# Optimization experiments

Measured on AMD Instinct MI355X. Metric: run time of the kernel, lower is better.

The kernel has to match this reference:

```python
import jax, jax.numpy as jnp
import numpy as np

N_NODES = 50000
N_EDGES = 800000
IN_F = 256
HID = 64
N_CLASSES = 32
LEAKY_SLOPE = 0.2


def _gat_layer(x, src, dst, W, a_src, a_dst):
    # Standard single-head GAT (GraphAttentionLayer_P0 semantics):
    # h = x W; e_ij = LeakyReLU(a_src.h_j + a_dst.h_i); softmax over in-edges of i;
    # out_i = sum_j alpha_ij h_j
    h = x @ W                                        # [N, F']
    alpha_s = h @ a_src                              # [N]
    alpha_d = h @ a_dst                              # [N]
    e = jax.nn.leaky_relu(alpha_s[src] + alpha_d[dst], LEAKY_SLOPE)  # [E]
    # segment softmax over edges grouped by destination node
    m = jax.ops.segment_max(e, dst, num_segments=N_NODES)           # [N]
    m = jnp.where(jnp.isfinite(m), m, 0.0)            # empty segments -> -inf
    ex = jnp.exp(e - m[dst])                          # [E]
    denom = jax.ops.segment_sum(ex, dst, num_segments=N_NODES)       # [N]
    denom = jnp.where(denom == 0.0, 1.0, denom)
    alpha = ex / denom[dst]                           # [E]
    out = jax.ops.segment_sum(alpha[:, None] * h[src], dst, num_segments=N_NODES)
    return out                                        # [N, F']


def setup_inputs() -> dict:
    key = jax.random.key(0)
    ks = jax.random.split(key, 8)
    x = jax.random.normal(ks[0], (N_NODES, IN_F), dtype=jnp.float32)
    edge_index = jax.random.randint(ks[1], (2, N_EDGES), 0, N_NODES, dtype=jnp.int64)
    s1 = 1.0 / np.sqrt(IN_F)
    s2 = 1.0 / np.sqrt(HID)
    W1 = jax.random.uniform(ks[2], (IN_F, HID), jnp.float32, -s1, s1)
    a1_src = jax.random.uniform(ks[3], (HID,), jnp.float32, -s2, s2)
    a1_dst = jax.random.uniform(ks[4], (HID,), jnp.float32, -s2, s2)
    W2 = jax.random.uniform(ks[5], (HID, N_CLASSES), jnp.float32, -s2, s2)
    s3 = 1.0 / np.sqrt(N_CLASSES)
    a2_src = jax.random.uniform(ks[6], (N_CLASSES,), jnp.float32, -s3, s3)
    a2_dst = jax.random.uniform(ks[7], (N_CLASSES,), jnp.float32, -s3, s3)
    return {"x": x, "edge_index": edge_index, "W1": W1, "a1_src": a1_src,
            "a1_dst": a1_dst, "W2": W2, "a2_src": a2_src, "a2_dst": a2_dst}


def reference(x, edge_index, W1, a1_src, a1_dst, W2, a2_src, a2_dst):
    src, dst = edge_index[0], edge_index[1]
    h = _gat_layer(x, src, dst, W1, a1_src, a1_dst)
    h = jax.nn.relu(h)
    out = _gat_layer(h, src, dst, W2, a2_src, a2_dst)
    return out
```

## Files before the change

### kernel.cpp

```cpp
#include <hip/hip_runtime.h>
#include <math.h>

#define NN 50000
#define NE 800000
#define INF_DIM 256
#define HIDF 64
#define NC 32
#define SLOPE 0.2f


__global__ void k_zero(int* __restrict__ counts){
  int i = blockIdx.x*blockDim.x + threadIdx.x;
  if(i < NN) counts[i] = 0;
}

__global__ void k_hist(const int* __restrict__ dst, int* __restrict__ counts){
  int e = blockIdx.x*blockDim.x + threadIdx.x;
  if(e < NE) atomicAdd(&counts[dst[e]], 1);
}

__global__ void k_scan_a(const int* __restrict__ counts, int* __restrict__ rowstart,
                         int* __restrict__ blocksums){
  __shared__ int wsum[4];
  int tid = threadIdx.x;
  int idx = blockIdx.x*1024 + tid*4;
  int v0 = (idx+0<NN)?counts[idx+0]:0;
  int v1 = (idx+1<NN)?counts[idx+1]:0;
  int v2 = (idx+2<NN)?counts[idx+2]:0;
  int v3 = (idx+3<NN)?counts[idx+3]:0;
  int s0=v0, s1=s0+v1, s2=s1+v2, s3=s2+v3;
  int lane = tid & 63, w = tid >> 6;
  int x = s3;
  #pragma unroll
  for(int off=1; off<64; off<<=1){
    int y = __shfl_up(x, off, 64);
    if(lane >= off) x += y;
  }
  if(lane==63) wsum[w] = x;
  __syncthreads();
  int woff = 0;
  for(int i=0;i<w;i++) woff += wsum[i];
  int excl = woff + (x - s3);
  if(idx+0<NN) rowstart[idx+1] = excl + s0;
  if(idx+1<NN) rowstart[idx+2] = excl + s1;
  if(idx+2<NN) rowstart[idx+3] = excl + s2;
  if(idx+3<NN) rowstart[idx+4] = excl + s3;
  if(tid==0) blocksums[blockIdx.x] = wsum[0]+wsum[1]+wsum[2]+wsum[3];
}

__global__ void k_scan_b(const int* __restrict__ blocksums, int* __restrict__ blockoff){
  int lane = threadIdx.x;
  const int nb = (NN + 1023)/1024;
  int v = (lane<nb)? blocksums[lane] : 0;
  int x = v;
  #pragma unroll
  for(int off=1; off<64; off<<=1){
    int y = __shfl_up(x, off, 64);
    if(lane >= off) x += y;
  }
  if(lane<nb) blockoff[lane] = x - v;
}

__global__ void k_scan_c(const int* __restrict__ counts, int* __restrict__ rowstart,
                         const int* __restrict__ blockoff, int* __restrict__ cursor){
  int i = blockIdx.x*blockDim.x + threadIdx.x;
  if(i < NN){
    int incl = rowstart[i+1] + blockoff[i>>10];
    rowstart[i+1] = incl;
    cursor[i] = incl - counts[i];
    if(i==0) rowstart[0] = 0;
  }
}

__global__ void k_scatter(const int* __restrict__ src, const int* __restrict__ dst,
                          int* __restrict__ cursor, int* __restrict__ ssrc){
  int e = blockIdx.x*blockDim.x + threadIdx.x;
  if(e < NE){
    int d = dst[e];
    int pos = atomicAdd(&cursor[d], 1);
    ssrc[pos] = src[e];
  }
}


__global__ __launch_bounds__(64) void k_gemm1(
    const float* __restrict__ x, const float* __restrict__ W,
    const float* __restrict__ a_s, const float* __restrict__ a_d,
    float* __restrict__ h, float* __restrict__ as_o, float* __restrict__ ad_o){
  __shared__ float ws[8*64];
  float4* wsv = reinterpret_cast<float4*>(ws);
  const float4* Wv = reinterpret_cast<const float4*>(W);
  int tid = threadIdx.x;
  int ng = tid >> 3, cg = tid & 7;
  int nb0 = blockIdx.x*32;

  const float* xrow[4];
  #pragma unroll
  for(int i=0;i<4;i++){
    int n = nb0 + ng + 8*i;
    xrow[i] = x + (size_t)((n < NN) ? n : (NN-1))*INF_DIM;
  }

  float4 acc[4][2];
  #pragma unroll
  for(int i=0;i<4;i++){ acc[i][0]=make_float4(0.f,0.f,0.f,0.f); acc[i][1]=make_float4(0.f,0.f,0.f,0.f); }

  for(int st=0; st<32; ++st){
    int k0 = st*8;
    wsv[tid]      = Wv[k0*16 + tid];
    wsv[tid + 64] = Wv[k0*16 + 64 + tid];
    float4 xa[4][2];
    #pragma unroll
    for(int i=0;i<4;i++){
      xa[i][0] = *reinterpret_cast<const float4*>(xrow[i] + k0);
      xa[i][1] = *reinterpret_cast<const float4*>(xrow[i] + k0 + 4);
    }
    __syncthreads();
    #pragma unroll
    for(int k4=0;k4<2;k4++){
      float4 wf[4][2];
      #pragma unroll
      for(int kk=0;kk<4;kk++){
        wf[kk][0] = wsv[(k4*4+kk)*16 + cg*2];
        wf[kk][1] = wsv[(k4*4+kk)*16 + cg*2 + 1];
      }
      #pragma unroll
      for(int i=0;i<4;i++){
        float4 xv = xa[i][k4];
        acc[i][0].x += xv.x*wf[0][0].x + xv.y*wf[1][0].x + xv.z*wf[2][0].x + xv.w*wf[3][0].x;
        acc[i][0].y += xv.x*wf[0][0].y + xv.y*wf[1][0].y + xv.z*wf[2][0].y + xv.w*wf[3][0].y;
        acc[i][0].z += xv.x*wf[0][0].z + xv.y*wf[1][0].z + xv.z*wf[2][0].z + xv.w*wf[3][0].z;
        acc[i][0].w += xv.x*wf[0][0].w + xv.y*wf[1][0].w + xv.z*wf[2][0].w + xv.w*wf[3][0].w;
        acc[i][1].x += xv.x*wf[0][1].x + xv.y*wf[1][1].x + xv.z*wf[2][1].x + xv.w*wf[3][1].x;
        acc[i][1].y += xv.x*wf[0][1].y + xv.y*wf[1][1].y + xv.z*wf[2][1].y + xv.w*wf[3][1].y;
        acc[i][1].z += xv.x*wf[0][1].z + xv.y*wf[1][1].z + xv.z*wf[2][1].z + xv.w*wf[3][1].z;
        acc[i][1].w += xv.x*wf[0][1].w + xv.y*wf[1][1].w + xv.z*wf[2][1].w + xv.w*wf[3][1].w;
      }
    }
    __syncthreads();
  }

  const float4* asv = reinterpret_cast<const float4*>(a_s);
  const float4* adv = reinterpret_cast<const float4*>(a_d);
  float4 asA = asv[cg*2], asB = asv[cg*2+1];
  float4 adA = adv[cg*2], adB = adv[cg*2+1];
  #pragma unroll
  for(int i=0;i<4;i++){
    int n = nb0 + ng + 8*i;
    float sv = acc[i][0].x*asA.x + acc[i][0].y*asA.y + acc[i][0].z*asA.z + acc[i][0].w*asA.w
             + acc[i][1].x*asB.x + acc[i][1].y*asB.y + acc[i][1].z*asB.z + acc[i][1].w*asB.w;
    float dv = acc[i][0].x*adA.x + acc[i][0].y*adA.y + acc[i][0].z*adA.z + acc[i][0].w*adA.w
             + acc[i][1].x*adB.x + acc[i][1].y*adB.y + acc[i][1].z*adB.z + acc[i][1].w*adB.w;
    #pragma unroll
    for(int mk=1; mk<8; mk<<=1){
      sv += __shfl_xor(sv, mk, 64);
      dv += __shfl_xor(dv, mk, 64);
    }
    if(n < NN){
      *reinterpret_cast<float4*>(h + (size_t)n*HIDF + cg*8)     = acc[i][0];
      *reinterpret_cast<float4*>(h + (size_t)n*HIDF + cg*8 + 4) = acc[i][1];
      if(cg==0){ as_o[n]=sv; ad_o[n]=dv; }
    }
  }
}


__global__ __launch_bounds__(256) void k_agg1(
    const float* __restrict__ h1, const float* __restrict__ as1, const float* __restrict__ ad1,
    const int* __restrict__ rowstart, const int* __restrict__ ssrc,
    float* __restrict__ r1){
  int lane = threadIdx.x & 63;
  int n = blockIdx.x*4 + (threadIdx.x >> 6);
  int rs = rowstart[n], re = rowstart[n+1];
  float adn = ad1[n];
  float m = -1e30f, l = 0.f, acc = 0.f;
  for(int base=rs; base<re; base+=64){
    int cnt = re - base; if(cnt > 64) cnt = 64;
    int s = 0; float z = -1e30f;
    if(lane < cnt){
      s = ssrc[base+lane];
      float zz = as1[s] + adn;
      z = zz > 0.f ? zz : SLOPE*zz;
    }
    float cm = z;
    #pragma unroll
    for(int off=32; off>=1; off>>=1) cm = fmaxf(cm, __shfl_xor(cm, off, 64));
    float nm = fmaxf(m, cm);
    float sc = __expf(m - nm);
    float p = (lane<cnt) ? __expf(z - nm) : 0.f;
    float cs = p;
    #pragma unroll
    for(int off=32; off>=1; off>>=1) cs += __shfl_xor(cs, off, 64);
    l = l*sc + cs;
    acc *= sc;
    int e = 0;
    for(; e+4<=cnt; e+=4){
      int   se0 = __shfl(s, e,   64), se1 = __shfl(s, e+1, 64);
      int   se2 = __shfl(s, e+2, 64), se3 = __shfl(s, e+3, 64);
      float pe0 = __shfl(p, e,   64), pe1 = __shfl(p, e+1, 64);
      float pe2 = __shfl(p, e+2, 64), pe3 = __shfl(p, e+3, 64);
      float v0 = h1[(size_t)se0*HIDF + lane];
      float v1 = h1[(size_t)se1*HIDF + lane];
      float v2 = h1[(size_t)se2*HIDF + lane];
      float v3 = h1[(size_t)se3*HIDF + lane];
      acc += pe0*v0; acc += pe1*v1; acc += pe2*v2; acc += pe3*v3;
    }
    for(; e<cnt; ++e){
      int   se = __shfl(s, e, 64);
      float pe = __shfl(p, e, 64);
      acc += pe * h1[(size_t)se*HIDF + lane];
    }
    m = nm;
  }
  float o = (l > 0.f) ? acc/l : 0.f;
  r1[(size_t)n*HIDF + lane] = fmaxf(o, 0.f);
}


__global__ __launch_bounds__(64) void k_gemm2(
    const float* __restrict__ r1, const float* __restrict__ W2,
    const float* __restrict__ a_s, const float* __restrict__ a_d,
    float* __restrict__ h2, float* __restrict__ as_o, float* __restrict__ ad_o){
  __shared__ float ws2[64*32];
  float4* wsv = reinterpret_cast<float4*>(ws2);
  const float4* Wv = reinterpret_cast<const float4*>(W2);
  int tid = threadIdx.x;
  int ng = tid >> 3, cg = tid & 7;
  int nb0 = blockIdx.x*32;
  #pragma unroll
  for(int j=0;j<8;j++) wsv[j*64 + tid] = Wv[j*64 + tid];

  const float* xrow[4];
  #pragma unroll
  for(int i=0;i<4;i++){
    int n = nb0 + ng + 8*i;
    xrow[i] = r1 + (size_t)((n < NN) ? n : (NN-1))*HIDF;
  }
  float4 acc[4];
  #pragma unroll
  for(int i=0;i<4;i++) acc[i] = make_float4(0.f,0.f,0.f,0.f);
  __syncthreads();

  for(int st=0; st<8; ++st){
    int k0 = st*8;
    float4 xa[4][2];
    #pragma unroll
    for(int i=0;i<4;i++){
      xa[i][0] = *reinterpret_cast<const float4*>(xrow[i] + k0);
      xa[i][1] = *reinterpret_cast<const float4*>(xrow[i] + k0 + 4);
    }
    #pragma unroll
    for(int k4=0;k4<2;k4++){
      float4 wf[4];
      #pragma unroll
      for(int kk=0;kk<4;kk++) wf[kk] = wsv[(k0 + k4*4 + kk)*8 + cg];
      #pragma unroll
      for(int i=0;i<4;i++){
        float4 xv = xa[i][k4];
        acc[i].x += xv.x*wf[0].x + xv.y*wf[1].x + xv.z*wf[2].x + xv.w*wf[3].x;
        acc[i].y += xv.x*wf[0].y + xv.y*wf[1].y + xv.z*wf[2].y + xv.w*wf[3].y;
        acc[i].z += xv.x*wf[0].z + xv.y*wf[1].z + xv.z*wf[2].z + xv.w*wf[3].z;
        acc[i].w += xv.x*wf[0].w + xv.y*wf[1].w + xv.z*wf[2].w + xv.w*wf[3].w;
      }
    }
  }

  const float4* asv = reinterpret_cast<const float4*>(a_s);
  const float4* adv = reinterpret_cast<const float4*>(a_d);
  float4 as4 = asv[cg], ad4 = adv[cg];
  #pragma unroll
  for(int i=0;i<4;i++){
    int n = nb0 + ng + 8*i;
    float sv = acc[i].x*as4.x + acc[i].y*as4.y + acc[i].z*as4.z + acc[i].w*as4.w;
    float dv = acc[i].x*ad4.x + acc[i].y*ad4.y + acc[i].z*ad4.z + acc[i].w*ad4.w;
    #pragma unroll
    for(int mk=1; mk<8; mk<<=1){
      sv += __shfl_xor(sv, mk, 64);
      dv += __shfl_xor(dv, mk, 64);
    }
    if(n < NN){
      *reinterpret_cast<float4*>(h2 + (size_t)n*NC + cg*4) = acc[i];
      if(cg==0){ as_o[n]=sv; ad_o[n]=dv; }
    }
  }
}


__global__ __launch_bounds__(256) void k_agg2(
    const float* __restrict__ h2, const float* __restrict__ as2, const float* __restrict__ ad2,
    const int* __restrict__ rowstart, const int* __restrict__ ssrc,
    float* __restrict__ out){
  int tid = threadIdx.x;
  int c = tid & 31;
  int n = blockIdx.x*8 + (tid >> 5);
  int rs = rowstart[n], re = rowstart[n+1];
  float adn = ad2[n];
  float m = -1e30f, l = 0.f, acc = 0.f;
  for(int base=rs; base<re; base+=32){
    int cnt = re - base; if(cnt > 32) cnt = 32;
    int s = 0; float z = -1e30f;
    if(c < cnt){
      s = ssrc[base+c];
      float zz = as2[s] + adn;
      z = zz > 0.f ? zz : SLOPE*zz;
    }
    float cm = z;
    #pragma unroll
    for(int off=16; off>=1; off>>=1) cm = fmaxf(cm, __shfl_xor(cm, off, 32));
    float nm = fmaxf(m, cm);
    float sc = __expf(m - nm);
    float p = (c<cnt) ? __expf(z - nm) : 0.f;
    float cs = p;
    #pragma unroll
    for(int off=16; off>=1; off>>=1) cs += __shfl_xor(cs, off, 32);
    l = l*sc + cs;
    acc *= sc;
    int e = 0;
    for(; e+4<=cnt; e+=4){
      int   se0 = __shfl(s, e,   32), se1 = __shfl(s, e+1, 32);
      int   se2 = __shfl(s, e+2, 32), se3 = __shfl(s, e+3, 32);
      float pe0 = __shfl(p, e,   32), pe1 = __shfl(p, e+1, 32);
      float pe2 = __shfl(p, e+2, 32), pe3 = __shfl(p, e+3, 32);
      float v0 = h2[(size_t)se0*NC + c];
      float v1 = h2[(size_t)se1*NC + c];
      float v2 = h2[(size_t)se2*NC + c];
      float v3 = h2[(size_t)se3*NC + c];
      acc += pe0*v0; acc += pe1*v1; acc += pe2*v2; acc += pe3*v3;
    }
    for(; e<cnt; ++e){
      int   se = __shfl(s, e, 32);
      float pe = __shfl(p, e, 32);
      acc += pe * h2[(size_t)se*NC + c];
    }
    m = nm;
  }
  out[(size_t)n*NC + c] = (l > 0.f) ? acc/l : 0.f;
}


extern "C" void kernel_launch(void* const* d_in, const int* in_sizes, int n_in,
                              void* d_out, int out_size, void* d_ws, size_t ws_size,
                              hipStream_t stream){
  const float* x   = (const float*)d_in[0];
  const int*   ei  = (const int*)d_in[1];
  const float* W1  = (const float*)d_in[2];
  const float* a1s = (const float*)d_in[3];
  const float* a1d = (const float*)d_in[4];
  const float* W2  = (const float*)d_in[5];
  const float* a2s = (const float*)d_in[6];
  const float* a2d = (const float*)d_in[7];
  const int* srcIdx = ei;
  const int* dstIdx = ei + NE;
  float* out = (float*)d_out;

  char* wsp = (char*)d_ws;
  size_t off = 0;
  auto alloc = [&](size_t bytes)->void*{
    void* p = wsp + off;
    off = (off + bytes + 255) & ~(size_t)255;
    return p;
  };
  int* counts    = (int*)alloc((size_t)NN*sizeof(int));
  int* rowstart  = (int*)alloc((size_t)(NN+1)*sizeof(int));
  int* cursor    = (int*)alloc((size_t)NN*sizeof(int));
  int* blocksums = (int*)alloc(64*sizeof(int));
  int* blockoff  = (int*)alloc(64*sizeof(int));
  int* ssrc      = (int*)alloc((size_t)NE*sizeof(int));
  float* h1      = (float*)alloc((size_t)NN*HIDF*sizeof(float));
  float* as1     = (float*)alloc((size_t)NN*sizeof(float));
  float* ad1     = (float*)alloc((size_t)NN*sizeof(float));
  float* r1      = (float*)alloc((size_t)NN*HIDF*sizeof(float));
  float* h2  = h1;
  float* as2 = as1;
  float* ad2 = ad1;

  k_zero   <<<(NN+255)/256, 256, 0, stream>>>(counts);
  k_hist   <<<(NE+255)/256, 256, 0, stream>>>(dstIdx, counts);
  k_scan_a <<<(NN+1023)/1024, 256, 0, stream>>>(counts, rowstart, blocksums);
  k_scan_b <<<1, 64, 0, stream>>>(blocksums, blockoff);
  k_scan_c <<<(NN+255)/256, 256, 0, stream>>>(counts, rowstart, blockoff, cursor);
  k_scatter<<<(NE+255)/256, 256, 0, stream>>>(srcIdx, dstIdx, cursor, ssrc);

  k_gemm1<<<(NN+31)/32, 64, 0, stream>>>(x, W1, a1s, a1d, h1, as1, ad1);
  k_agg1 <<<NN/4, 256, 0, stream>>>(h1, as1, ad1, rowstart, ssrc, r1);

  k_gemm2<<<(NN+31)/32, 64, 0, stream>>>(r1, W2, a2s, a2d, h2, as2, ad2);
  k_agg2 <<<NN/8, 256, 0, stream>>>(h2, as2, ad2, rowstart, ssrc, out);
}
```

Before: 302.7 us.

## Rewrite projection GEMMs with register-prefetched weights instead of shared memory

Both dense projection kernels drop the shared-memory weight staging and its barriers. Each thread now reads its weight slice straight from global or cache into a rotating register window, and prefetches x rows two steps ahead in double-buffered registers. Blocks now cover 16 nodes instead of 32, which doubles the grid but halves the rows each thread handles. This removes syncthreads stalls but adds redundant global weight loads per wave, and the extra clamped loads at the end of the weight stream could raise cache traffic.

```diff
diff --git a/kernel.cpp b/kernel.cpp
--- a/kernel.cpp
+++ b/kernel.cpp
@@ -7,6 +7,14 @@
 #define HIDF 64
 #define NC 32
 #define SLOPE 0.2f
+
+__device__ __forceinline__ float elem8(const float4& a, const float4& b, int kk){
+  switch(kk){
+    case 0: return a.x; case 1: return a.y; case 2: return a.z; case 3: return a.w;
+    case 4: return b.x; case 5: return b.y; case 6: return b.z; default: return b.w;
+  }
+}
+#define FMA4(A,S,V) {A.x += (S)*(V).x; A.y += (S)*(V).y; A.z += (S)*(V).z; A.w += (S)*(V).w;}
 
 
 __global__ void k_zero(int* __restrict__ counts){
@@ -87,80 +95,84 @@
     const float* __restrict__ x, const float* __restrict__ W,
     const float* __restrict__ a_s, const float* __restrict__ a_d,
     float* __restrict__ h, float* __restrict__ as_o, float* __restrict__ ad_o){
-  __shared__ float ws[8*64];
-  float4* wsv = reinterpret_cast<float4*>(ws);
-  const float4* Wv = reinterpret_cast<const float4*>(W);
-  int tid = threadIdx.x;
-  int ng = tid >> 3, cg = tid & 7;
-  int nb0 = blockIdx.x*32;
-
-  const float* xrow[4];
-  #pragma unroll
-  for(int i=0;i<4;i++){
-    int n = nb0 + ng + 8*i;
-    xrow[i] = x + (size_t)((n < NN) ? n : (NN-1))*INF_DIM;
-  }
-
-  float4 acc[4][2];
-  #pragma unroll
-  for(int i=0;i<4;i++){ acc[i][0]=make_float4(0.f,0.f,0.f,0.f); acc[i][1]=make_float4(0.f,0.f,0.f,0.f); }
-
+  int lane = threadIdx.x;
+  int cg = lane & 7;
+  int ng = lane >> 3;
+  int nb0 = blockIdx.x*16;
+  int n0 = nb0 + ng, n1 = nb0 + ng + 8;
+  const float* xr0 = x + (size_t)(n0 < NN ? n0 : NN-1)*INF_DIM;
+  const float* xr1 = x + (size_t)(n1 < NN ? n1 : NN-1)*INF_DIM;
+  const float* wp = W + cg*8;
+
+  float4 acc00 = make_float4(0.f,0.f,0.f,0.f), acc01 = acc00;
+  float4 acc10 = acc00, acc11 = acc00;
+
+  float4 xs[2][2][2];
+  float4 wr[4][2];
+
+  #pragma unroll
+  for(int s=0;s<2;s++){
+    xs[s][0][0] = *(const float4*)(xr0 + s*8);
+    xs[s][0][1] = *(const float4*)(xr0 + s*8 + 4);
+    xs[s][1][0] = *(const float4*)(xr1 + s*8);
+    xs[s][1][1] = *(const float4*)(xr1 + s*8 + 4);
+  }
+  #pragma unroll
+  for(int r=0;r<4;r++){
+    wr[r][0] = *(const float4*)(wp + r*64);
+    wr[r][1] = *(const float4*)(wp + r*64 + 4);
+  }
+
+  #pragma unroll 2
   for(int st=0; st<32; ++st){
-    int k0 = st*8;
-    wsv[tid]      = Wv[k0*16 + tid];
-    wsv[tid + 64] = Wv[k0*16 + 64 + tid];
-    float4 xa[4][2];
-    #pragma unroll
-    for(int i=0;i<4;i++){
-      xa[i][0] = *reinterpret_cast<const float4*>(xrow[i] + k0);
-      xa[i][1] = *reinterpret_cast<const float4*>(xrow[i] + k0 + 4);
-    }
-    __syncthreads();
-    #pragma unroll
-    for(int k4=0;k4<2;k4++){
-      float4 wf[4][2];
-      #pragma unroll
-      for(int kk=0;kk<4;kk++){
-        wf[kk][0] = wsv[(k4*4+kk)*16 + cg*2];
-        wf[kk][1] = wsv[(k4*4+kk)*16 + cg*2 + 1];
-      }
-      #pragma unroll
-      for(int i=0;i<4;i++){
-        float4 xv = xa[i][k4];
-        acc[i][0].x += xv.x*wf[0][0].x + xv.y*wf[1][0].x + xv.z*wf[2][0].x + xv.w*wf[3][0].x;
-        acc[i][0].y += xv.x*wf[0][0].y + xv.y*wf[1][0].y + xv.z*wf[2][0].y + xv.w*wf[3][0].y;
-        acc[i][0].z += xv.x*wf[0][0].z + xv.y*wf[1][0].z + xv.z*wf[2][0].z + xv.w*wf[3][0].z;
-        acc[i][0].w += xv.x*wf[0][0].w + xv.y*wf[1][0].w + xv.z*wf[2][0].w + xv.w*wf[3][0].w;
-        acc[i][1].x += xv.x*wf[0][1].x + xv.y*wf[1][1].x + xv.z*wf[2][1].x + xv.w*wf[3][1].x;
-        acc[i][1].y += xv.x*wf[0][1].y + xv.y*wf[1][1].y + xv.z*wf[2][1].y + xv.w*wf[3][1].y;
-        acc[i][1].z += xv.x*wf[0][1].z + xv.y*wf[1][1].z + xv.z*wf[2][1].z + xv.w*wf[3][1].z;
-        acc[i][1].w += xv.x*wf[0][1].w + xv.y*wf[1][1].w + xv.z*wf[2][1].w + xv.w*wf[3][1].w;
-      }
-    }
-    __syncthreads();
-  }
-
-  const float4* asv = reinterpret_cast<const float4*>(a_s);
-  const float4* adv = reinterpret_cast<const float4*>(a_d);
-  float4 asA = asv[cg*2], asB = asv[cg*2+1];
-  float4 adA = adv[cg*2], adB = adv[cg*2+1];
-  #pragma unroll
-  for(int i=0;i<4;i++){
-    int n = nb0 + ng + 8*i;
-    float sv = acc[i][0].x*asA.x + acc[i][0].y*asA.y + acc[i][0].z*asA.z + acc[i][0].w*asA.w
-             + acc[i][1].x*asB.x + acc[i][1].y*asB.y + acc[i][1].z*asB.z + acc[i][1].w*asB.w;
-    float dv = acc[i][0].x*adA.x + acc[i][0].y*adA.y + acc[i][0].z*adA.z + acc[i][0].w*adA.w
-             + acc[i][1].x*adB.x + acc[i][1].y*adB.y + acc[i][1].z*adB.z + acc[i][1].w*adB.w;
-    #pragma unroll
-    for(int mk=1; mk<8; mk<<=1){
-      sv += __shfl_xor(sv, mk, 64);
-      dv += __shfl_xor(dv, mk, 64);
-    }
-    if(n < NN){
-      *reinterpret_cast<float4*>(h + (size_t)n*HIDF + cg*8)     = acc[i][0];
-      *reinterpret_cast<float4*>(h + (size_t)n*HIDF + cg*8 + 4) = acc[i][1];
-      if(cg==0){ as_o[n]=sv; ad_o[n]=dv; }
-    }
+    int buf = st & 1;
+    #pragma unroll
+    for(int kk=0; kk<8; ++kk){
+      float xk0 = elem8(xs[buf][0][0], xs[buf][0][1], kk);
+      float xk1 = elem8(xs[buf][1][0], xs[buf][1][1], kk);
+      float4 wa = wr[kk & 3][0];
+      float4 wb = wr[kk & 3][1];
+      FMA4(acc00, xk0, wa) FMA4(acc01, xk0, wb)
+      FMA4(acc10, xk1, wa) FMA4(acc11, xk1, wb)
+      int knext = st*8 + kk + 4; if(knext > 255) knext = 255;
+      wr[kk & 3][0] = *(const float4*)(wp + knext*64);
+      wr[kk & 3][1] = *(const float4*)(wp + knext*64 + 4);
+    }
+    int sn = st + 2;
+    if(sn < 32){
+      xs[buf][0][0] = *(const float4*)(xr0 + sn*8);
+      xs[buf][0][1] = *(const float4*)(xr0 + sn*8 + 4);
+      xs[buf][1][0] = *(const float4*)(xr1 + sn*8);
+      xs[buf][1][1] = *(const float4*)(xr1 + sn*8 + 4);
+    }
+  }
+
+  float4 asA = *(const float4*)(a_s + cg*8), asB = *(const float4*)(a_s + cg*8 + 4);
+  float4 adA = *(const float4*)(a_d + cg*8), adB = *(const float4*)(a_d + cg*8 + 4);
+  float sv0 = acc00.x*asA.x + acc00.y*asA.y + acc00.z*asA.z + acc00.w*asA.w
+            + acc01.x*asB.x + acc01.y*asB.y + acc01.z*asB.z + acc01.w*asB.w;
+  float dv0 = acc00.x*adA.x + acc00.y*adA.y + acc00.z*adA.z + acc00.w*adA.w
+            + acc01.x*adB.x + acc01.y*adB.y + acc01.z*adB.z + acc01.w*adB.w;
+  float sv1 = acc10.x*asA.x + acc10.y*asA.y + acc10.z*asA.z + acc10.w*asA.w
+            + acc11.x*asB.x + acc11.y*asB.y + acc11.z*asB.z + acc11.w*asB.w;
+  float dv1 = acc10.x*adA.x + acc10.y*adA.y + acc10.z*adA.z + acc10.w*adA.w
+            + acc11.x*adB.x + acc11.y*adB.y + acc11.z*adB.z + acc11.w*adB.w;
+  #pragma unroll
+  for(int mk=1; mk<8; mk<<=1){
+    sv0 += __shfl_xor(sv0, mk, 64);
+    dv0 += __shfl_xor(dv0, mk, 64);
+    sv1 += __shfl_xor(sv1, mk, 64);
+    dv1 += __shfl_xor(dv1, mk, 64);
+  }
+  if(n0 < NN){
+    *(float4*)(h + (size_t)n0*HIDF + cg*8)     = acc00;
+    *(float4*)(h + (size_t)n0*HIDF + cg*8 + 4) = acc01;
+    if(cg==0){ as_o[n0]=sv0; ad_o[n0]=dv0; }
+  }
+  if(n1 < NN){
+    *(float4*)(h + (size_t)n1*HIDF + cg*8)     = acc10;
+    *(float4*)(h + (size_t)n1*HIDF + cg*8 + 4) = acc11;
+    if(cg==0){ as_o[n1]=sv1; ad_o[n1]=dv1; }
   }
 }
 
@@ -221,67 +233,63 @@
     const float* __restrict__ r1, const float* __restrict__ W2,
     const float* __restrict__ a_s, const float* __restrict__ a_d,
     float* __restrict__ h2, float* __restrict__ as_o, float* __restrict__ ad_o){
-  __shared__ float ws2[64*32];
-  float4* wsv = reinterpret_cast<float4*>(ws2);
-  const float4* Wv = reinterpret_cast<const float4*>(W2);
-  int tid = threadIdx.x;
-  int ng = tid >> 3, cg = tid & 7;
-  int nb0 = blockIdx.x*32;
-  #pragma unroll
-  for(int j=0;j<8;j++) wsv[j*64 + tid] = Wv[j*64 + tid];
-
-  const float* xrow[4];
-  #pragma unroll
-  for(int i=0;i<4;i++){
-    int n = nb0 + ng + 8*i;
-    xrow[i] = r1 + (size_t)((n < NN) ? n : (NN-1))*HIDF;
-  }
-  float4 acc[4];
-  #pragma unroll
-  for(int i=0;i<4;i++) acc[i] = make_float4(0.f,0.f,0.f,0.f);
-  __syncthreads();
-
+  int lane = threadIdx.x;
+  int cg = lane & 3;
+  int ng = lane >> 2;
+  int n = blockIdx.x*16 + ng;
+  const float* xrow = r1 + (size_t)(n < NN ? n : NN-1)*HIDF;
+  const float* wp = W2 + cg*8;
+
+  float4 acc0 = make_float4(0.f,0.f,0.f,0.f), acc1 = acc0;
+  float4 xs[2][2];
+  float4 wr[4][2];
+
+  #pragma unroll
+  for(int s=0;s<2;s++){
+    xs[s][0] = *(const float4*)(xrow + s*8);
+    xs[s][1] = *(const float4*)(xrow + s*8 + 4);
+  }
+  #pragma unroll
+  for(int r=0;r<4;r++){
+    wr[r][0] = *(const float4*)(wp + r*32);
+    wr[r][1] = *(const float4*)(wp + r*32 + 4);
+  }
+
+  #pragma unroll 2
   for(int st=0; st<8; ++st){
-    int k0 = st*8;
-    float4 xa[4][2];
-    #pragma unroll
-    for(int i=0;i<4;i++){
-      xa[i][0] = *reinterpret_cast<const float4*>(xrow[i] + k0);
-      xa[i][1] = *reinterpret_cast<const float4*>(xrow[i] + k0 + 4);
-    }
-    #pragma unroll
-    for(int k4=0;k4<2;k4++){
-      float4 wf[4];
-      #pragma unroll
-      for(int kk=0;kk<4;kk++) wf[kk] = wsv[(k0 + k4*4 + kk)*8 + cg];
-      #pragma unroll
-      for(int i=0;i<4;i++){
-        float4 xv = xa[i][k4];
-        acc[i].x += xv.x*wf[0].x + xv.y*wf[1].x + xv.z*wf[2].x + xv.w*wf[3].x;
-        acc[i].y += xv.x*wf[0].y + xv.y*wf[1].y + xv.z*wf[2].y + xv.w*wf[3].y;
-        acc[i].z += xv.x*wf[0].z + xv.y*wf[1].z + xv.z*wf[2].z + xv.w*wf[3].z;
-        acc[i].w += xv.x*wf[0].w + xv.y*wf[1].w + xv.z*wf[2].w + xv.w*wf[3].w;
-      }
-    }
-  }
-
-  const float4* asv = reinterpret_cast<const float4*>(a_s);
-  const float4* adv = reinterpret_cast<const float4*>(a_d);
-  float4 as4 = asv[cg], ad4 = adv[cg];
-  #pragma unroll
-  for(int i=0;i<4;i++){
-    int n = nb0 + ng + 8*i;
-    float sv = acc[i].x*as4.x + acc[i].y*as4.y + acc[i].z*as4.z + acc[i].w*as4.w;
-    float dv = acc[i].x*ad4.x + acc[i].y*ad4.y + acc[i].z*ad4.z + acc[i].w*ad4.w;
-    #pragma unroll
-    for(int mk=1; mk<8; mk<<=1){
-      sv += __shfl_xor(sv, mk, 64);
-      dv += __shfl_xor(dv, mk, 64);
-    }
-    if(n < NN){
-      *reinterpret_cast<float4*>(h2 + (size_t)n*NC + cg*4) = acc[i];
-      if(cg==0){ as_o[n]=sv; ad_o[n]=dv; }
-    }
+    int buf = st & 1;
+    #pragma unroll
+    for(int kk=0; kk<8; ++kk){
+      float xk = elem8(xs[buf][0], xs[buf][1], kk);
+      float4 wa = wr[kk & 3][0];
+      float4 wb = wr[kk & 3][1];
+      FMA4(acc0, xk, wa) FMA4(acc1, xk, wb)
+      int knext = st*8 + kk + 4; if(knext > 63) knext = 63;
+      wr[kk & 3][0] = *(const float4*)(wp + knext*32);
+      wr[kk & 3][1] = *(const float4*)(wp + knext*32 + 4);
+    }
+    int sn = st + 2;
+    if(sn < 8){
+      xs[buf][0] = *(const float4*)(xrow + sn*8);
+      xs[buf][1] = *(const float4*)(xrow + sn*8 + 4);
+    }
+  }
+
+  float4 asA = *(const float4*)(a_s + cg*8), asB = *(const float4*)(a_s + cg*8 + 4);
+  float4 adA = *(const float4*)(a_d + cg*8), adB = *(const float4*)(a_d + cg*8 + 4);
+  float sv = acc0.x*asA.x + acc0.y*asA.y + acc0.z*asA.z + acc0.w*asA.w
+           + acc1.x*asB.x + acc1.y*asB.y + acc1.z*asB.z + acc1.w*asB.w;
+  float dv = acc0.x*adA.x + acc0.y*adA.y + acc0.z*adA.z + acc0.w*adA.w
+           + acc1.x*adB.x + acc1.y*adB.y + acc1.z*adB.z + acc1.w*adB.w;
+  #pragma unroll
+  for(int mk=1; mk<4; mk<<=1){
+    sv += __shfl_xor(sv, mk, 64);
+    dv += __shfl_xor(dv, mk, 64);
+  }
+  if(n < NN){
+    *(float4*)(h2 + (size_t)n*NC + cg*8)     = acc0;
+    *(float4*)(h2 + (size_t)n*NC + cg*8 + 4) = acc1;
+    if(cg==0){ as_o[n]=sv; ad_o[n]=dv; }
   }
 }
 
@@ -381,9 +389,9 @@
   k_scan_c <<<(NN+255)/256, 256, 0, stream>>>(counts, rowstart, blockoff, cursor);
   k_scatter<<<(NE+255)/256, 256, 0, stream>>>(srcIdx, dstIdx, cursor, ssrc);
 
-  k_gemm1<<<(NN+31)/32, 64, 0, stream>>>(x, W1, a1s, a1d, h1, as1, ad1);
+  k_gemm1<<<(NN+15)/16, 64, 0, stream>>>(x, W1, a1s, a1d, h1, as1, ad1);
   k_agg1 <<<NN/4, 256, 0, stream>>>(h1, as1, ad1, rowstart, ssrc, r1);
 
-  k_gemm2<<<(NN+31)/32, 64, 0, stream>>>(r1, W2, a2s, a2d, h2, as2, ad2);
+  k_gemm2<<<(NN+15)/16, 64, 0, stream>>>(r1, W2, a2s, a2d, h2, as2, ad2);
   k_agg2 <<<NN/8, 256, 0, stream>>>(h2, as2, ad2, rowstart, ssrc, out);
 }
```

Result: slower. 346.5 us (+14.5%).

## Restructure both GEMMs to one output column per lane with register double-buffering

Applied to the files above, without the earlier changes.

Both projection GEMMs are rewritten so each lane owns one output column and accumulates 8 node rows. X rows are broadcast float4 loads shared across the wavefront, and W columns are read directly from global memory, replacing the LDS staging and its barriers. The next k-slice is prefetched into registers while the current one is computed. This removes shared-memory traffic and syncs, but makes the attention dot-products use full-wave shuffle reductions and relies on NN being divisible by 8 and 16.

```diff
diff --git a/kernel.cpp b/kernel.cpp
--- a/kernel.cpp
+++ b/kernel.cpp
@@ -7,6 +7,10 @@
 #define HIDF 64
 #define NC 32
 #define SLOPE 0.2f
+
+__device__ __forceinline__ float elem4(const float4& v, int kk){
+  switch(kk){ case 0: return v.x; case 1: return v.y; case 2: return v.z; default: return v.w; }
+}
 
 
 __global__ void k_zero(int* __restrict__ counts){
@@ -87,80 +91,53 @@
     const float* __restrict__ x, const float* __restrict__ W,
     const float* __restrict__ a_s, const float* __restrict__ a_d,
     float* __restrict__ h, float* __restrict__ as_o, float* __restrict__ ad_o){
-  __shared__ float ws[8*64];
-  float4* wsv = reinterpret_cast<float4*>(ws);
-  const float4* Wv = reinterpret_cast<const float4*>(W);
-  int tid = threadIdx.x;
-  int ng = tid >> 3, cg = tid & 7;
-  int nb0 = blockIdx.x*32;
-
-  const float* xrow[4];
-  #pragma unroll
-  for(int i=0;i<4;i++){
-    int n = nb0 + ng + 8*i;
-    xrow[i] = x + (size_t)((n < NN) ? n : (NN-1))*INF_DIM;
-  }
-
-  float4 acc[4][2];
-  #pragma unroll
-  for(int i=0;i<4;i++){ acc[i][0]=make_float4(0.f,0.f,0.f,0.f); acc[i][1]=make_float4(0.f,0.f,0.f,0.f); }
-
-  for(int st=0; st<32; ++st){
-    int k0 = st*8;
-    wsv[tid]      = Wv[k0*16 + tid];
-    wsv[tid + 64] = Wv[k0*16 + 64 + tid];
-    float4 xa[4][2];
-    #pragma unroll
-    for(int i=0;i<4;i++){
-      xa[i][0] = *reinterpret_cast<const float4*>(xrow[i] + k0);
-      xa[i][1] = *reinterpret_cast<const float4*>(xrow[i] + k0 + 4);
-    }
-    __syncthreads();
-    #pragma unroll
-    for(int k4=0;k4<2;k4++){
-      float4 wf[4][2];
-      #pragma unroll
-      for(int kk=0;kk<4;kk++){
-        wf[kk][0] = wsv[(k4*4+kk)*16 + cg*2];
-        wf[kk][1] = wsv[(k4*4+kk)*16 + cg*2 + 1];
-      }
-      #pragma unroll
-      for(int i=0;i<4;i++){
-        float4 xv = xa[i][k4];
-        acc[i][0].x += xv.x*wf[0][0].x + xv.y*wf[1][0].x + xv.z*wf[2][0].x + xv.w*wf[3][0].x;
-        acc[i][0].y += xv.x*wf[0][0].y + xv.y*wf[1][0].y + xv.z*wf[2][0].y + xv.w*wf[3][0].y;
-        acc[i][0].z += xv.x*wf[0][0].z + xv.y*wf[1][0].z + xv.z*wf[2][0].z + xv.w*wf[3][0].z;
-        acc[i][0].w += xv.x*wf[0][0].w + xv.y*wf[1][0].w + xv.z*wf[2][0].w + xv.w*wf[3][0].w;
-        acc[i][1].x += xv.x*wf[0][1].x + xv.y*wf[1][1].x + xv.z*wf[2][1].x + xv.w*wf[3][1].x;
-        acc[i][1].y += xv.x*wf[0][1].y + xv.y*wf[1][1].y + xv.z*wf[2][1].y + xv.w*wf[3][1].y;
-        acc[i][1].z += xv.x*wf[0][1].z + xv.y*wf[1][1].z + xv.z*wf[2][1].z + xv.w*wf[3][1].z;
-        acc[i][1].w += xv.x*wf[0][1].w + xv.y*wf[1][1].w + xv.z*wf[2][1].w + xv.w*wf[3][1].w;
-      }
-    }
-    __syncthreads();
-  }
-
-  const float4* asv = reinterpret_cast<const float4*>(a_s);
-  const float4* adv = reinterpret_cast<const float4*>(a_d);
-  float4 asA = asv[cg*2], asB = asv[cg*2+1];
-  float4 adA = adv[cg*2], adB = adv[cg*2+1];
-  #pragma unroll
-  for(int i=0;i<4;i++){
-    int n = nb0 + ng + 8*i;
-    float sv = acc[i][0].x*asA.x + acc[i][0].y*asA.y + acc[i][0].z*asA.z + acc[i][0].w*asA.w
-             + acc[i][1].x*asB.x + acc[i][1].y*asB.y + acc[i][1].z*asB.z + acc[i][1].w*asB.w;
-    float dv = acc[i][0].x*adA.x + acc[i][0].y*adA.y + acc[i][0].z*adA.z + acc[i][0].w*adA.w
-             + acc[i][1].x*adB.x + acc[i][1].y*adB.y + acc[i][1].z*adB.z + acc[i][1].w*adB.w;
-    #pragma unroll
-    for(int mk=1; mk<8; mk<<=1){
+  int c = threadIdx.x;
+  int nb = blockIdx.x*8;
+  const float* wc = W + c;
+
+  float acc[8];
+  #pragma unroll
+  for(int i=0;i<8;i++) acc[i] = 0.f;
+
+  float4 xs[2][8];
+  float  wr[2][4];
+
+  #pragma unroll
+  for(int i=0;i<8;i++) xs[0][i] = *(const float4*)(x + (size_t)(nb+i)*INF_DIM);
+  #pragma unroll
+  for(int kk=0;kk<4;kk++) wr[0][kk] = wc[kk*64];
+
+  #pragma unroll 2
+  for(int st=0; st<64; ++st){
+    int buf = st & 1, nxt = buf ^ 1;
+    if(st < 63){
+      int k0 = (st+1)*4;
+      #pragma unroll
+      for(int i=0;i<8;i++)
+        xs[nxt][i] = *(const float4*)(x + (size_t)(nb+i)*INF_DIM + k0);
+      #pragma unroll
+      for(int kk=0;kk<4;kk++) wr[nxt][kk] = wc[(k0+kk)*64];
+    }
+    #pragma unroll
+    for(int kk=0;kk<4;kk++){
+      float w = wr[buf][kk];
+      #pragma unroll
+      for(int i=0;i<8;i++) acc[i] += elem4(xs[buf][i], kk) * w;
+    }
+  }
+
+  float asc = a_s[c], adc = a_d[c];
+  #pragma unroll
+  for(int i=0;i<8;i++){
+    int n = nb + i;
+    h[(size_t)n*HIDF + c] = acc[i];
+    float sv = acc[i]*asc, dv = acc[i]*adc;
+    #pragma unroll
+    for(int mk=1; mk<64; mk<<=1){
       sv += __shfl_xor(sv, mk, 64);
       dv += __shfl_xor(dv, mk, 64);
     }
-    if(n < NN){
-      *reinterpret_cast<float4*>(h + (size_t)n*HIDF + cg*8)     = acc[i][0];
-      *reinterpret_cast<float4*>(h + (size_t)n*HIDF + cg*8 + 4) = acc[i][1];
-      if(cg==0){ as_o[n]=sv; ad_o[n]=dv; }
-    }
+    if(c==0){ as_o[n]=sv; ad_o[n]=dv; }
   }
 }
 
@@ -221,67 +198,55 @@
     const float* __restrict__ r1, const float* __restrict__ W2,
     const float* __restrict__ a_s, const float* __restrict__ a_d,
     float* __restrict__ h2, float* __restrict__ as_o, float* __restrict__ ad_o){
-  __shared__ float ws2[64*32];
-  float4* wsv = reinterpret_cast<float4*>(ws2);
-  const float4* Wv = reinterpret_cast<const float4*>(W2);
-  int tid = threadIdx.x;
-  int ng = tid >> 3, cg = tid & 7;
-  int nb0 = blockIdx.x*32;
-  #pragma unroll
-  for(int j=0;j<8;j++) wsv[j*64 + tid] = Wv[j*64 + tid];
-
-  const float* xrow[4];
-  #pragma unroll
-  for(int i=0;i<4;i++){
-    int n = nb0 + ng + 8*i;
-    xrow[i] = r1 + (size_t)((n < NN) ? n : (NN-1))*HIDF;
-  }
-  float4 acc[4];
-  #pragma unroll
-  for(int i=0;i<4;i++) acc[i] = make_float4(0.f,0.f,0.f,0.f);
-  __syncthreads();
-
-  for(int st=0; st<8; ++st){
-    int k0 = st*8;
-    float4 xa[4][2];
-    #pragma unroll
-    for(int i=0;i<4;i++){
-      xa[i][0] = *reinterpret_cast<const float4*>(xrow[i] + k0);
-      xa[i][1] = *reinterpret_cast<const float4*>(xrow[i] + k0 + 4);
-    }
-    #pragma unroll
-    for(int k4=0;k4<2;k4++){
-      float4 wf[4];
-      #pragma unroll
-      for(int kk=0;kk<4;kk++) wf[kk] = wsv[(k0 + k4*4 + kk)*8 + cg];
-      #pragma unroll
-      for(int i=0;i<4;i++){
-        float4 xv = xa[i][k4];
-        acc[i].x += xv.x*wf[0].x + xv.y*wf[1].x + xv.z*wf[2].x + xv.w*wf[3].x;
-        acc[i].y += xv.x*wf[0].y + xv.y*wf[1].y + xv.z*wf[2].y + xv.w*wf[3].y;
-        acc[i].z += xv.x*wf[0].z + xv.y*wf[1].z + xv.z*wf[2].z + xv.w*wf[3].z;
-        acc[i].w += xv.x*wf[0].w + xv.y*wf[1].w + xv.z*wf[2].w + xv.w*wf[3].w;
-      }
-    }
-  }
-
-  const float4* asv = reinterpret_cast<const float4*>(a_s);
-  const float4* adv = reinterpret_cast<const float4*>(a_d);
-  float4 as4 = asv[cg], ad4 = adv[cg];
-  #pragma unroll
-  for(int i=0;i<4;i++){
-    int n = nb0 + ng + 8*i;
-    float sv = acc[i].x*as4.x + acc[i].y*as4.y + acc[i].z*as4.z + acc[i].w*as4.w;
-    float dv = acc[i].x*ad4.x + acc[i].y*ad4.y + acc[i].z*ad4.z + acc[i].w*ad4.w;
-    #pragma unroll
-    for(int mk=1; mk<8; mk<<=1){
+  int lane = threadIdx.x;
+  int c = lane & 31;
+  int g = lane >> 5;
+  int nb = blockIdx.x*16 + g*8;
+  const float* wc = W2 + c;
+
+  float acc[8];
+  #pragma unroll
+  for(int i=0;i<8;i++) acc[i] = 0.f;
+
+  float4 xs[2][8];
+  float  wr[2][4];
+
+  #pragma unroll
+  for(int i=0;i<8;i++) xs[0][i] = *(const float4*)(r1 + (size_t)(nb+i)*HIDF);
+  #pragma unroll
+  for(int kk=0;kk<4;kk++) wr[0][kk] = wc[kk*32];
+
+  #pragma unroll 2
+  for(int st=0; st<16; ++st){
+    int buf = st & 1, nxt = buf ^ 1;
+    if(st < 15){
+      int k0 = (st+1)*4;
+      #pragma unroll
+      for(int i=0;i<8;i++)
+        xs[nxt][i] = *(const float4*)(r1 + (size_t)(nb+i)*HIDF + k0);
+      #pragma unroll
+      for(int kk=0;kk<4;kk++) wr[nxt][kk] = wc[(k0+kk)*32];
+    }
+    #pragma unroll
+    for(int kk=0;kk<4;kk++){
+      float w = wr[buf][kk];
+      #pragma unroll
+      for(int i=0;i<8;i++) acc[i] += elem4(xs[buf][i], kk) * w;
+    }
+  }
+
+  float asc = a_s[c], adc = a_d[c];
+  #pragma unroll
+  for(int i=0;i<8;i++){
+    int n = nb + i;
+    h2[(size_t)n*NC + c] = acc[i];
+    float sv = acc[i]*asc, dv = acc[i]*adc;
+    #pragma unroll
+    for(int mk=1; mk<32; mk<<=1){
       sv += __shfl_xor(sv, mk, 64);
       dv += __shfl_xor(dv, mk, 64);
     }
-    if(n < NN){
-      *reinterpret_cast<float4*>(h2 + (size_t)n*NC + cg*4) = acc[i];
-      if(cg==0){ as_o[n]=sv; ad_o[n]=dv; }
-    }
+    if(c==0){ as_o[n]=sv; ad_o[n]=dv; }
   }
 }
 
@@ -381,9 +346,9 @@
   k_scan_c <<<(NN+255)/256, 256, 0, stream>>>(counts, rowstart, blockoff, cursor);
   k_scatter<<<(NE+255)/256, 256, 0, stream>>>(srcIdx, dstIdx, cursor, ssrc);
 
-  k_gemm1<<<(NN+31)/32, 64, 0, stream>>>(x, W1, a1s, a1d, h1, as1, ad1);
+  k_gemm1<<<NN/8, 64, 0, stream>>>(x, W1, a1s, a1d, h1, as1, ad1);
   k_agg1 <<<NN/4, 256, 0, stream>>>(h1, as1, ad1, rowstart, ssrc, r1);
 
-  k_gemm2<<<(NN+31)/32, 64, 0, stream>>>(r1, W2, a2s, a2d, h2, as2, ad2);
+  k_gemm2<<<NN/16, 64, 0, stream>>>(r1, W2, a2s, a2d, h2, as2, ad2);
   k_agg2 <<<NN/8, 256, 0, stream>>>(h2, as2, ad2, rowstart, ssrc, out);
 }
```

Result: slower. 388.2 us (+28.2%).

## Double-buffer GEMM tiles, prefetch x rows, and unroll aggregation gathers by eight

Applied to the files above, without the earlier changes.

k_gemm1 now keeps two W tiles in LDS and loads the next one while computing on the current one. It drops both __syncthreads, on the basis that the 64-thread block is a single wave64. Both GEMMs also prefetch x rows two K-steps ahead in registers, and their dot products are rewritten as explicit scalar-times-vector FMAs. The aggregation kernels unroll the neighbor gather loop from 4 to 8 so more independent loads are in flight, at the cost of extra registers and a longer scalar tail loop.

```diff
diff --git a/kernel.cpp b/kernel.cpp
--- a/kernel.cpp
+++ b/kernel.cpp
@@ -7,6 +7,11 @@
 #define HIDF 64
 #define NC 32
 #define SLOPE 0.2f
+
+__device__ __forceinline__ float elem4(const float4& v, int kk){
+  switch(kk){ case 0: return v.x; case 1: return v.y; case 2: return v.z; default: return v.w; }
+}
+#define FMA4(A,S,V) {A.x += (S)*(V).x; A.y += (S)*(V).y; A.z += (S)*(V).z; A.w += (S)*(V).w;}
 
 
 __global__ void k_zero(int* __restrict__ counts){
@@ -87,7 +92,7 @@
     const float* __restrict__ x, const float* __restrict__ W,
     const float* __restrict__ a_s, const float* __restrict__ a_d,
     float* __restrict__ h, float* __restrict__ as_o, float* __restrict__ ad_o){
-  __shared__ float ws[8*64];
+  __shared__ float ws[2*8*64];
   float4* wsv = reinterpret_cast<float4*>(ws);
   const float4* Wv = reinterpret_cast<const float4*>(W);
   int tid = threadIdx.x;
@@ -105,39 +110,55 @@
   #pragma unroll
   for(int i=0;i<4;i++){ acc[i][0]=make_float4(0.f,0.f,0.f,0.f); acc[i][1]=make_float4(0.f,0.f,0.f,0.f); }
 
+  {
+    float4 wa = Wv[tid], wb = Wv[64+tid];
+    wsv[tid] = wa; wsv[64+tid] = wb;
+  }
+  float4 xs[2][4][2];
+  #pragma unroll
+  for(int i=0;i<4;i++){
+    xs[0][i][0] = *(const float4*)(xrow[i]);
+    xs[0][i][1] = *(const float4*)(xrow[i] + 4);
+    xs[1][i][0] = *(const float4*)(xrow[i] + 8);
+    xs[1][i][1] = *(const float4*)(xrow[i] + 12);
+  }
+
+  #pragma unroll 2
   for(int st=0; st<32; ++st){
-    int k0 = st*8;
-    wsv[tid]      = Wv[k0*16 + tid];
-    wsv[tid + 64] = Wv[k0*16 + 64 + tid];
-    float4 xa[4][2];
-    #pragma unroll
-    for(int i=0;i<4;i++){
-      xa[i][0] = *reinterpret_cast<const float4*>(xrow[i] + k0);
-      xa[i][1] = *reinterpret_cast<const float4*>(xrow[i] + k0 + 4);
-    }
-    __syncthreads();
-    #pragma unroll
-    for(int k4=0;k4<2;k4++){
+    int cur = st & 1, nxt = cur ^ 1;
+    if(st < 31){
+      float4 wa = Wv[(st+1)*128 + tid];
+      float4 wb = Wv[(st+1)*128 + 64 + tid];
+      wsv[nxt*128 + tid] = wa;
+      wsv[nxt*128 + 64 + tid] = wb;
+    }
+    #pragma unroll
+    for(int g=0; g<2; ++g){
       float4 wf[4][2];
       #pragma unroll
       for(int kk=0;kk<4;kk++){
-        wf[kk][0] = wsv[(k4*4+kk)*16 + cg*2];
-        wf[kk][1] = wsv[(k4*4+kk)*16 + cg*2 + 1];
+        wf[kk][0] = wsv[cur*128 + (g*4+kk)*16 + cg*2];
+        wf[kk][1] = wsv[cur*128 + (g*4+kk)*16 + cg*2 + 1];
       }
       #pragma unroll
       for(int i=0;i<4;i++){
-        float4 xv = xa[i][k4];
-        acc[i][0].x += xv.x*wf[0][0].x + xv.y*wf[1][0].x + xv.z*wf[2][0].x + xv.w*wf[3][0].x;
-        acc[i][0].y += xv.x*wf[0][0].y + xv.y*wf[1][0].y + xv.z*wf[2][0].y + xv.w*wf[3][0].y;
-        acc[i][0].z += xv.x*wf[0][0].z + xv.y*wf[1][0].z + xv.z*wf[2][0].z + xv.w*wf[3][0].z;
-        acc[i][0].w += xv.x*wf[0][0].w + xv.y*wf[1][0].w + xv.z*wf[2][0].w + xv.w*wf[3][0].w;
-        acc[i][1].x += xv.x*wf[0][1].x + xv.y*wf[1][1].x + xv.z*wf[2][1].x + xv.w*wf[3][1].x;
-        acc[i][1].y += xv.x*wf[0][1].y + xv.y*wf[1][1].y + xv.z*wf[2][1].y + xv.w*wf[3][1].y;
-        acc[i][1].z += xv.x*wf[0][1].z + xv.y*wf[1][1].z + xv.z*wf[2][1].z + xv.w*wf[3][1].z;
-        acc[i][1].w += xv.x*wf[0][1].w + xv.y*wf[1][1].w + xv.z*wf[2][1].w + xv.w*wf[3][1].w;
+        float4 xv = xs[cur][i][g];
+        #pragma unroll
+        for(int kk=0;kk<4;kk++){
+          float xk = elem4(xv, kk);
+          FMA4(acc[i][0], xk, wf[kk][0])
+          FMA4(acc[i][1], xk, wf[kk][1])
+        }
       }
     }
-    __syncthreads();
+    if(st < 30){
+      int k0 = (st+2)*8;
+      #pragma unroll
+      for(int i=0;i<4;i++){
+        xs[cur][i][0] = *(const float4*)(xrow[i] + k0);
+        xs[cur][i][1] = *(const float4*)(xrow[i] + k0 + 4);
+      }
+    }
   }
 
   const float4* asv = reinterpret_cast<const float4*>(a_s);
@@ -157,8 +178,8 @@
       dv += __shfl_xor(dv, mk, 64);
     }
     if(n < NN){
-      *reinterpret_cast<float4*>(h + (size_t)n*HIDF + cg*8)     = acc[i][0];
-      *reinterpret_cast<float4*>(h + (size_t)n*HIDF + cg*8 + 4) = acc[i][1];
+      *(float4*)(h + (size_t)n*HIDF + cg*8)     = acc[i][0];
+      *(float4*)(h + (size_t)n*HIDF + cg*8 + 4) = acc[i][1];
       if(cg==0){ as_o[n]=sv; ad_o[n]=dv; }
     }
   }
@@ -194,16 +215,14 @@
     l = l*sc + cs;
     acc *= sc;
     int e = 0;
-    for(; e+4<=cnt; e+=4){
-      int   se0 = __shfl(s, e,   64), se1 = __shfl(s, e+1, 64);
-      int   se2 = __shfl(s, e+2, 64), se3 = __shfl(s, e+3, 64);
-      float pe0 = __shfl(p, e,   64), pe1 = __shfl(p, e+1, 64);
-      float pe2 = __shfl(p, e+2, 64), pe3 = __shfl(p, e+3, 64);
-      float v0 = h1[(size_t)se0*HIDF + lane];
-      float v1 = h1[(size_t)se1*HIDF + lane];
-      float v2 = h1[(size_t)se2*HIDF + lane];
-      float v3 = h1[(size_t)se3*HIDF + lane];
-      acc += pe0*v0; acc += pe1*v1; acc += pe2*v2; acc += pe3*v3;
+    for(; e+8<=cnt; e+=8){
+      int se[8]; float pe[8], v[8];
+      #pragma unroll
+      for(int u=0;u<8;u++){ se[u] = __shfl(s, e+u, 64); pe[u] = __shfl(p, e+u, 64); }
+      #pragma unroll
+      for(int u=0;u<8;u++) v[u] = h1[(size_t)se[u]*HIDF + lane];
+      #pragma unroll
+      for(int u=0;u<8;u++) acc += pe[u]*v[u];
     }
     for(; e<cnt; ++e){
       int   se = __shfl(s, e, 64);
@@ -239,28 +258,41 @@
   float4 acc[4];
   #pragma unroll
   for(int i=0;i<4;i++) acc[i] = make_float4(0.f,0.f,0.f,0.f);
-  __syncthreads();
-
+
+  float4 xs[2][4][2];
+  #pragma unroll
+  for(int i=0;i<4;i++){
+    xs[0][i][0] = *(const float4*)(xrow[i]);
+    xs[0][i][1] = *(const float4*)(xrow[i] + 4);
+    xs[1][i][0] = *(const float4*)(xrow[i] + 8);
+    xs[1][i][1] = *(const float4*)(xrow[i] + 12);
+  }
+
+  #pragma unroll 2
   for(int st=0; st<8; ++st){
+    int cur = st & 1;
     int k0 = st*8;
-    float4 xa[4][2];
-    #pragma unroll
-    for(int i=0;i<4;i++){
-      xa[i][0] = *reinterpret_cast<const float4*>(xrow[i] + k0);
-      xa[i][1] = *reinterpret_cast<const float4*>(xrow[i] + k0 + 4);
-    }
-    #pragma unroll
-    for(int k4=0;k4<2;k4++){
+    #pragma unroll
+    for(int g=0; g<2; ++g){
       float4 wf[4];
       #pragma unroll
-      for(int kk=0;kk<4;kk++) wf[kk] = wsv[(k0 + k4*4 + kk)*8 + cg];
+      for(int kk=0;kk<4;kk++) wf[kk] = wsv[(k0 + g*4 + kk)*8 + cg];
       #pragma unroll
       for(int i=0;i<4;i++){
-        float4 xv = xa[i][k4];
-        acc[i].x += xv.x*wf[0].x + xv.y*wf[1].x + xv.z*wf[2].x + xv.w*wf[3].x;
-        acc[i].y += xv.x*wf[0].y + xv.y*wf[1].y + xv.z*wf[2].y + xv.w*wf[3].y;
-        acc[i].z += xv.x*wf[0].z + xv.y*wf[1].z + xv.z*wf[2].z + xv.w*wf[3].z;
-        acc[i].w += xv.x*wf[0].w + xv.y*wf[1].w + xv.z*wf[2].w + xv.w*wf[3].w;
+        float4 xv = xs[cur][i][g];
+        #pragma unroll
+        for(int kk=0;kk<4;kk++){
+          float xk = elem4(xv, kk);
+          FMA4(acc[i], xk, wf[kk])
+        }
+      }
+    }
+    if(st < 6){
+      int kn = (st+2)*8;
+      #pragma unroll
+      for(int i=0;i<4;i++){
+        xs[cur][i][0] = *(const float4*)(xrow[i] + kn);
+        xs[cur][i][1] = *(const float4*)(xrow[i] + kn + 4);
       }
     }
   }
@@ -279,7 +311,7 @@
       dv += __shfl_xor(dv, mk, 64);
     }
     if(n < NN){
-      *reinterpret_cast<float4*>(h2 + (size_t)n*NC + cg*4) = acc[i];
+      *(float4*)(h2 + (size_t)n*NC + cg*4) = acc[i];
       if(cg==0){ as_o[n]=sv; ad_o[n]=dv; }
     }
   }
@@ -316,16 +348,14 @@
     l = l*sc + cs;
     acc *= sc;
     int e = 0;
-    for(; e+4<=cnt; e+=4){
-      int   se0 = __shfl(s, e,   32), se1 = __shfl(s, e+1, 32);
-      int   se2 = __shfl(s, e+2, 32), se3 = __shfl(s, e+3, 32);
-      float pe0 = __shfl(p, e,   32), pe1 = __shfl(p, e+1, 32);
-      float pe2 = __shfl(p, e+2, 32), pe3 = __shfl(p, e+3, 32);
-      float v0 = h2[(size_t)se0*NC + c];
-      float v1 = h2[(size_t)se1*NC + c];
-      float v2 = h2[(size_t)se2*NC + c];
-      float v3 = h2[(size_t)se3*NC + c];
-      acc += pe0*v0; acc += pe1*v1; acc += pe2*v2; acc += pe3*v3;
+    for(; e+8<=cnt; e+=8){
+      int se[8]; float pe[8], v[8];
+      #pragma unroll
+      for(int u=0;u<8;u++){ se[u] = __shfl(s, e+u, 32); pe[u] = __shfl(p, e+u, 32); }
+      #pragma unroll
+      for(int u=0;u<8;u++) v[u] = h2[(size_t)se[u]*NC + c];
+      #pragma unroll
+      for(int u=0;u<8;u++) acc += pe[u]*v[u];
     }
     for(; e<cnt; ++e){
       int   se = __shfl(s, e, 32);
```

Result: no change. 305.4 us (+0.9%).
